# Optimization experiments

Hardware: AMD Instinct MI355X
Metric: run time of the kernel (lower is better)

## Reference

```python
import jax, jax.numpy as jnp
import numpy as np

B, SQ, SKV, D, H = 4, 2048, 2048, 1024, 16
DH = D // H  # 64


def setup_inputs() -> dict:
    key = jax.random.key(0)
    ks = jax.random.split(key, 8)
    s = 0.02  # realistic init scale for weights
    return {
        "query": jax.random.normal(ks[0], (B, SQ, D), dtype=jnp.float32),
        "value": jax.random.normal(ks[1], (B, SKV, D), dtype=jnp.float32),
        "wq": jax.random.normal(ks[2], (H, D, DH), dtype=jnp.float32) * s,
        "bq": jnp.zeros((H, DH), dtype=jnp.float32),
        "wk": jax.random.normal(ks[3], (H, D, DH), dtype=jnp.float32) * s,
        "bk": jnp.zeros((H, DH), dtype=jnp.float32),
        "wv": jax.random.normal(ks[4], (H, D, DH), dtype=jnp.float32) * s,
        "bv": jnp.zeros((H, DH), dtype=jnp.float32),
        "wo": jax.random.normal(ks[5], (D, D), dtype=jnp.float32) * s,
        "bo": jnp.zeros((D,), dtype=jnp.float32),
    }


def reference(query, value, wq, bq, wk, bk, wv, bv, wo, bo):
    # Batched equivalent of the per-head Dense loop: [B,S,D] x [H,D,DH] -> [B,H,S,DH]
    q = jnp.einsum("bsd,hde->bhse", query, wq) + bq[None, :, None, :]
    k = jnp.einsum("bsd,hde->bhse", value, wk) + bk[None, :, None, :]
    v = jnp.einsum("bsd,hde->bhse", value, wv) + bv[None, :, None, :]
    scale = 1.0 / jnp.sqrt(jnp.asarray(DH, dtype=q.dtype))
    scores = jnp.einsum("bhqe,bhke->bhqk", q, k) * scale  # [B,H,SQ,SKV]
    align = jax.nn.softmax(scores, axis=-1)
    heads = jnp.einsum("bhqk,bhke->bhqe", align, v)  # [B,H,SQ,DH]
    # concat heads along feature dim (head order preserved)
    heads = jnp.transpose(heads, (0, 2, 1, 3)).reshape(B, SQ, D)
    return heads @ wo + bo
```

## Files before the change

kernel.cpp:

```cpp
#include <hip/hip_runtime.h>
#include <stdint.h>

#define DEVI __device__ __forceinline__

typedef __bf16  bf16x8 __attribute__((ext_vector_type(8)));
typedef float   f32x4  __attribute__((ext_vector_type(4)));
typedef float   f32x16 __attribute__((ext_vector_type(16)));
typedef uint32_t u32x4 __attribute__((ext_vector_type(4)));
typedef uint32_t u32x2v __attribute__((ext_vector_type(2)));
typedef uint16_t u16x8 __attribute__((ext_vector_type(8)));
typedef uint16_t u16x4 __attribute__((ext_vector_type(4)));

static constexpr int BB = 4, SQL = 2048, SKVL = 2048, DMODEL = 1024, NH = 16;
static constexpr int MROWS = BB * SQL;
static constexpr int KD = DMODEL;

DEVI uint16_t f2bf(float x) {
  uint32_t u = __builtin_bit_cast(uint32_t, x);
  u += 0x7FFFu + ((u >> 16) & 1u);
  return (uint16_t)(u >> 16);
}
DEVI uint32_t cvt2bf(float a, float b) {
  __bf16 x = (__bf16)a, y = (__bf16)b;
  return (uint32_t)__builtin_bit_cast(uint16_t, x) |
         ((uint32_t)__builtin_bit_cast(uint16_t, y) << 16);
}
DEVI f32x4 mfma16(bf16x8 a, bf16x8 b, f32x4 c) {
  return __builtin_amdgcn_mfma_f32_16x16x32_bf16(a, b, c, 0, 0, 0);
}
DEVI f32x16 mfma32(bf16x8 a, bf16x8 b, f32x16 c) {
  return __builtin_amdgcn_mfma_f32_32x32x16_bf16(a, b, c, 0, 0, 0);
}
DEVI void gload16(const void* g, void* l) {
  __builtin_amdgcn_global_load_lds((__attribute__((address_space(1))) const void*)g,
                                   (__attribute__((address_space(3))) void*)l, 16, 0, 0);
}
DEVI bf16x8 ldread(const void* p) { return __builtin_bit_cast(bf16x8, *(const u32x4*)p); }
DEVI u32x2v plswap(uint32_t a, uint32_t b) {
  return __builtin_amdgcn_permlane32_swap(a, b, false, false);
}

__global__ __launch_bounds__(256) void k_cvt_act(const float* __restrict__ q, const float* __restrict__ v,
                                                 uint16_t* __restrict__ aq, uint16_t* __restrict__ av) {
  const int64_t n4 = (int64_t)MROWS * DMODEL / 4;
  for (int64_t i = (int64_t)blockIdx.x * 256 + threadIdx.x; i < 2 * n4; i += (int64_t)gridDim.x * 256) {
    const bool second = (i >= n4);
    const int64_t j = second ? i - n4 : i;
    const float4 x = (second ? (const float4*)v : (const float4*)q)[j];
    u16x4 o = { f2bf(x.x), f2bf(x.y), f2bf(x.z), f2bf(x.w) };
    *(u16x4*)((second ? av : aq) + j * 4) = o;
  }
}

__global__ __launch_bounds__(256) void k_cvt_w(const float* __restrict__ wq, const float* __restrict__ wk,
                                               const float* __restrict__ wv, const float* __restrict__ wo,
                                               uint16_t* __restrict__ wt) {
  const int idx = blockIdx.x * 256 + threadIdx.x;
  const int z = idx >> 20, f = idx & 1048575;
  const int n = f >> 10, d = f & 1023;
  const float* w = (z == 0) ? wq : (z == 1) ? wk : (z == 2) ? wv : wo;
  const float x = (z < 3) ? w[((n >> 6) << 16) + d * 64 + (n & 63)] : w[d * 1024 + n];
  wt[(size_t)z * 1048576 + f] = f2bf(x);
}

template <int MODE>
__global__ __launch_bounds__(256) void k_gemm(const uint16_t* __restrict__ A, const uint16_t* __restrict__ Bt,
                                              const float* __restrict__ bias, const float* __restrict__ biasB,
                                              void* __restrict__ outp, void* __restrict__ outpB,
                                              float oscale) {
  __shared__ __align__(16) uint16_t Al[128 * 64];
  __shared__ __align__(16) uint16_t Bl[128 * 64];
  const int tid = threadIdx.x;
  const int w = tid >> 6, ln = tid & 63;
  const int g = ln >> 4, lc = ln & 15;
  const int m0 = blockIdx.x * 128, n0 = blockIdx.y * 128;
  const int wm = (w >> 1) * 64, wn = (w & 1) * 64;
  const int srow = w * 32 + (ln >> 3);
  const int colp = (ln & 7) * 16;

  f32x4 acc[4][4] = {};

  for (int kt = 0; kt < KD / 64; ++kt) {
    #pragma unroll
    for (int i = 0; i < 4; ++i) {
      const int row = srow + i * 8;
      const int colb = colp ^ ((row & 7) << 4);
      gload16((const char*)(A + (size_t)(m0 + row) * KD + kt * 64) + colb,
              (char*)Al + w * 4096 + i * 1024);
      gload16((const char*)(Bt + (size_t)(n0 + row) * KD + kt * 64) + colb,
              (char*)Bl + w * 4096 + i * 1024);
    }
    __syncthreads();
    #pragma unroll
    for (int kk = 0; kk < 2; ++kk) {
      bf16x8 af[4], bfr[4];
      #pragma unroll
      for (int mt = 0; mt < 4; ++mt) {
        const int row = wm + mt * 16 + lc;
        af[mt] = ldread((const char*)Al + row * 128 + ((kk * 64 + g * 16) ^ ((row & 7) << 4)));
      }
      #pragma unroll
      for (int nt = 0; nt < 4; ++nt) {
        const int row = wn + nt * 16 + lc;
        bfr[nt] = ldread((const char*)Bl + row * 128 + ((kk * 64 + g * 16) ^ ((row & 7) << 4)));
      }
      #pragma unroll
      for (int mt = 0; mt < 4; ++mt)
        #pragma unroll
        for (int nt = 0; nt < 4; ++nt)
          acc[mt][nt] = mfma16(af[mt], bfr[nt], acc[mt][nt]);
    }
    __syncthreads();
  }
  #pragma unroll
  for (int nt = 0; nt < 4; ++nt) {
    const int n = n0 + wn + nt * 16 + lc;
    const int z = (MODE == 2) ? (n >> 10) : 0;
    const int nn = (MODE == 2) ? (n & 1023) : n;
    const float bv = (MODE == 2) ? (z ? biasB : bias)[nn] : bias[n];
    uint16_t* dst16 = (uint16_t*)((MODE == 2 && z) ? outpB : outp);
    #pragma unroll
    for (int mt = 0; mt < 4; ++mt) {
      #pragma unroll
      for (int r = 0; r < 4; ++r) {
        const int m = m0 + wm + mt * 16 + g * 4 + r;
        if (MODE != 1) {
          float val = acc[mt][nt][r] + bv;
          if (MODE == 0) val *= oscale;
          const int b = m >> 11, s = m & 2047, h = nn >> 6, e = nn & 63;
          dst16[((size_t)((b * NH + h) * SQL + s)) * 64 + e] = f2bf(val);
        } else {
          ((float*)outp)[(size_t)m * DMODEL + n] = acc[mt][nt][r] + bv;
        }
      }
    }
  }
}

__global__ __launch_bounds__(256, 2) void k_attn(const uint16_t* __restrict__ Qb,
                                                 const uint16_t* __restrict__ Kb,
                                                 const uint16_t* __restrict__ Vb,
                                                 uint16_t* __restrict__ Hd) {
  __shared__ __align__(16) uint16_t Kl[2][64 * 64];
  __shared__ __align__(16) uint16_t Vl[2][64 * 64];
  const int tid = threadIdx.x;
  const int w = tid >> 6, ln = tid & 63;
  const int ql = ln & 31, hi = ln >> 5;
  const int bh = blockIdx.y;
  const int q0 = blockIdx.x * 256 + w * 64;

  bf16x8 qf[2][4];
  #pragma unroll
  for (int qt = 0; qt < 2; ++qt) {
    const uint16_t* Qp = Qb + ((size_t)bh * SQL + q0 + qt * 32 + ql) * 64;
    #pragma unroll
    for (int s = 0; s < 4; ++s)
      qf[qt][s] = __builtin_bit_cast(bf16x8, *(const u16x8*)(Qp + s * 16 + hi * 8));
  }

  const uint16_t* Kbase = Kb + (size_t)bh * SKVL * 64;
  const uint16_t* Vbase = Vb + (size_t)bh * SKVL * 64;

  const int swl = (ln & 7) << 4;
  const int e0off = (hi << 4) ^ swl;
  const int rb = ql * 128;

  const int krow0 = w * 16 + (ln >> 3);
  const int kcolb = (((ln & 7) ^ (ln >> 3)) << 4);
  const int vkv = (tid & 31) * 2, ve0 = (tid >> 5) * 8;

  f32x16 acc[2][2] = {};
  float lsum0 = 0.f, lsum1 = 0.f;

  {
    #pragma unroll
    for (int i = 0; i < 2; ++i) {
      const int row = krow0 + i * 8;
      gload16((const char*)(Kbase + (size_t)row * 64) + kcolb,
              (char*)&Kl[0][0] + w * 2048 + i * 1024);
    }
    const u16x8 a = *(const u16x8*)(Vbase + (size_t)vkv * 64 + ve0);
    const u16x8 b = *(const u16x8*)(Vbase + (size_t)(vkv + 1) * 64 + ve0);
    #pragma unroll
    for (int i = 0; i < 8; ++i) {
      const int e = ve0 + i;
      *(uint32_t*)((char*)&Vl[0][0] + e * 128 + ((vkv * 2) ^ ((e & 7) << 4))) =
          (uint32_t)a[i] | ((uint32_t)b[i] << 16);
    }
  }
  __syncthreads();

  int cur = 0;
  for (int t = 0; t < SKVL / 64; ++t) {
    const bool pre = (t + 1 < SKVL / 64);
    u16x8 nv0, nv1;
    if (pre) {
      const uint16_t* Kc = Kbase + (size_t)(t + 1) * 4096;
      #pragma unroll
      for (int i = 0; i < 2; ++i) {
        const int row = krow0 + i * 8;
        gload16((const char*)(Kc + (size_t)row * 64) + kcolb,
                (char*)&Kl[cur ^ 1][0] + w * 2048 + i * 1024);
      }
      const uint16_t* Vc = Vbase + (size_t)(t + 1) * 4096;
      nv0 = *(const u16x8*)(Vc + (size_t)vkv * 64 + ve0);
      nv1 = *(const u16x8*)(Vc + (size_t)(vkv + 1) * 64 + ve0);
    }
    const char* Kc0 = (const char*)&Kl[cur][0];
    uint32_t w32[2][2][4][2];
    #pragma unroll
    for (int qt = 0; qt < 2; ++qt) {
      f32x16 s0 = {}, s1 = {};
      __builtin_amdgcn_s_setprio(1);
      #pragma unroll
      for (int s = 0; s < 4; ++s) {
        const int off = e0off ^ (s << 5);
        const bf16x8 k0 = ldread(Kc0 + rb + off);
        const bf16x8 k1 = ldread(Kc0 + 4096 + rb + off);
        s0 = mfma32(k0, qf[qt][s], s0);
        s1 = mfma32(k1, qf[qt][s], s1);
      }
      __builtin_amdgcn_s_setprio(0);
      float ps = 0.f;
      #pragma unroll
      for (int r = 0; r < 16; ++r) {
        s0[r] = __builtin_amdgcn_exp2f(s0[r]);
        s1[r] = __builtin_amdgcn_exp2f(s1[r]);
        ps += s0[r] + s1[r];
      }
      if (qt == 0) lsum0 += ps; else lsum1 += ps;
      #pragma unroll
      for (int c8 = 0; c8 < 4; ++c8) {
        #pragma unroll
        for (int p = 0; p < 2; ++p) {
          w32[qt][0][c8][p] = cvt2bf(s0[4 * c8 + 2 * p], s0[4 * c8 + 2 * p + 1]);
          w32[qt][1][c8][p] = cvt2bf(s1[4 * c8 + 2 * p], s1[4 * c8 + 2 * p + 1]);
        }
      }
    }
    const char* Vc0 = (const char*)&Vl[cur][0];
    __builtin_amdgcn_s_setprio(1);
    #pragma unroll
    for (int u = 0; u < 4; ++u) {
      const int tt = u >> 1, ul = u & 1;
      const int off = e0off ^ (u << 5);
      const bf16x8 v0 = ldread(Vc0 + rb + off);
      const bf16x8 v1 = ldread(Vc0 + 4096 + rb + off);
      #pragma unroll
      for (int qt = 0; qt < 2; ++qt) {
        const u32x2v e0 = plswap(w32[qt][tt][2 * ul][0], w32[qt][tt][2 * ul + 1][0]);
        const u32x2v e1 = plswap(w32[qt][tt][2 * ul][1], w32[qt][tt][2 * ul + 1][1]);
        u32x4 pj;
        pj[0] = e0[0]; pj[1] = e1[0]; pj[2] = e0[1]; pj[3] = e1[1];
        const bf16x8 pb = __builtin_bit_cast(bf16x8, pj);
        acc[qt][0] = mfma32(v0, pb, acc[qt][0]);
        acc[qt][1] = mfma32(v1, pb, acc[qt][1]);
      }
    }
    __builtin_amdgcn_s_setprio(0);
    if (pre) {
      #pragma unroll
      for (int i = 0; i < 8; ++i) {
        const int e = ve0 + i;
        *(uint32_t*)((char*)&Vl[cur ^ 1][0] + e * 128 + ((vkv * 2) ^ ((e & 7) << 4))) =
            (uint32_t)nv0[i] | ((uint32_t)nv1[i] << 16);
      }
    }
    __syncthreads();
    cur ^= 1;
  }
  const int b = bh >> 4, h = bh & 15;
  #pragma unroll
  for (int qt = 0; qt < 2; ++qt) {
    const float ls = qt ? lsum1 : lsum0;
    const float lt = ls + __shfl_xor(ls, 32);
    const float inv = __builtin_amdgcn_rcpf(lt);
    uint16_t* op = Hd + ((size_t)(b * SQL + q0 + qt * 32 + ql)) * DMODEL + h * 64;
    #pragma unroll
    for (int et = 0; et < 2; ++et) {
      #pragma unroll
      for (int r2 = 0; r2 < 8; ++r2) {
        const float v0 = acc[qt][et][2 * r2] * inv;
        const float v1 = acc[qt][et][2 * r2 + 1] * inv;
        const int e = et * 32 + 4 * hi + (r2 & 1) * 2 + (r2 >> 1) * 8;
        *(uint32_t*)(op + e) = cvt2bf(v0, v1);
      }
    }
  }
}

extern "C" void kernel_launch(void* const* d_in, const int* in_sizes, int n_in,
                              void* d_out, int out_size, void* d_ws, size_t ws_size,
                              hipStream_t stream) {
  const float* query = (const float*)d_in[0];
  const float* value = (const float*)d_in[1];
  const float* wq = (const float*)d_in[2];
  const float* bq = (const float*)d_in[3];
  const float* wk = (const float*)d_in[4];
  const float* bk = (const float*)d_in[5];
  const float* wv = (const float*)d_in[6];
  const float* bv = (const float*)d_in[7];
  const float* wo = (const float*)d_in[8];
  const float* bo = (const float*)d_in[9];

  const size_t SZ_ACT = (size_t)MROWS * DMODEL * 2;
  const size_t SZ_W   = (size_t)4 * DMODEL * DMODEL * 2;
  if (ws_size < 6 * SZ_ACT + SZ_W) return;

  char* ws = (char*)d_ws;
  uint16_t* Aq = (uint16_t*)ws;  ws += SZ_ACT;
  uint16_t* Av = (uint16_t*)ws;  ws += SZ_ACT;
  uint16_t* Wt = (uint16_t*)ws;  ws += SZ_W;
  uint16_t* Qb = (uint16_t*)ws;  ws += SZ_ACT;
  uint16_t* Kb = (uint16_t*)ws;  ws += SZ_ACT;
  uint16_t* Vb = (uint16_t*)ws;  ws += SZ_ACT;
  uint16_t* Hd = (uint16_t*)ws;  ws += SZ_ACT;

  const float QSCALE = 0.18033688011112042f;

  k_cvt_act<<<dim3(2048), dim3(256), 0, stream>>>(query, value, Aq, Av);
  k_cvt_w<<<dim3(16384), dim3(256), 0, stream>>>(wq, wk, wv, wo, Wt);
  k_gemm<0><<<dim3(64, 8), dim3(256), 0, stream>>>(Aq, Wt, bq, nullptr, Qb, nullptr, QSCALE);
  k_gemm<2><<<dim3(64, 16), dim3(256), 0, stream>>>(Av, Wt + 1048576, bk, bv, Kb, Vb, 1.0f);
  k_attn<<<dim3(8, 64), dim3(256), 0, stream>>>(Qb, Kb, Vb, Hd);
  k_gemm<1><<<dim3(64, 8), dim3(256), 0, stream>>>(Hd, Wt + 3145728, bo, nullptr, d_out, nullptr, 1.0f);
}
```

Baseline: 220.8 us.

## Split attention KV range in two and merge partials in a combine kernel

The attention kernel now splits each (batch, head) KV sequence into two halves handled by separate blocks, doubling the grid to 1024 blocks. A swizzled 1D block index groups blocks for locality. Each block writes unnormalized bf16 partial outputs and row sums to scratch reused from dead workspace buffers (Aq/Av and Wt). A new k_comb kernel adds the two partials, normalizes them and writes the head-concatenated layout. The aim is higher occupancy and more in-flight work (launch bounds raised to 4 blocks per SM), at the cost of an extra kernel launch, extra memory traffic for the partials, bf16 rounding of the partials before summing, and possible register pressure.

```diff
diff --git a/kernel.cpp b/kernel.cpp
--- a/kernel.cpp
+++ b/kernel.cpp
@@ -20,6 +20,7 @@
   u += 0x7FFFu + ((u >> 16) & 1u);
   return (uint16_t)(u >> 16);
 }
+DEVI float bf2f(uint16_t x) { return __builtin_bit_cast(float, (uint32_t)x << 16); }
 DEVI uint32_t cvt2bf(float a, float b) {
   __bf16 x = (__bf16)a, y = (__bf16)b;
   return (uint32_t)__builtin_bit_cast(uint16_t, x) |
@@ -137,17 +138,20 @@
   }
 }
 
-__global__ __launch_bounds__(256, 2) void k_attn(const uint16_t* __restrict__ Qb,
+__global__ __launch_bounds__(256, 4) void k_attn(const uint16_t* __restrict__ Qb,
                                                  const uint16_t* __restrict__ Kb,
                                                  const uint16_t* __restrict__ Vb,
-                                                 uint16_t* __restrict__ Hd) {
+                                                 uint16_t* __restrict__ Op,
+                                                 float* __restrict__ Lp) {
   __shared__ __align__(16) uint16_t Kl[2][64 * 64];
   __shared__ __align__(16) uint16_t Vl[2][64 * 64];
   const int tid = threadIdx.x;
   const int w = tid >> 6, ln = tid & 63;
   const int ql = ln & 31, hi = ln >> 5;
-  const int bh = blockIdx.y;
-  const int q0 = blockIdx.x * 256 + w * 64;
+  const int bsw = blockIdx.x;
+  const int l = (bsw & 7) * 128 + (bsw >> 3);
+  const int qx = l & 7, bh = (l >> 3) & 63, z = l >> 9;
+  const int q0 = qx * 256 + w * 64;
 
   bf16x8 qf[2][4];
   #pragma unroll
@@ -158,8 +162,8 @@
       qf[qt][s] = __builtin_bit_cast(bf16x8, *(const u16x8*)(Qp + s * 16 + hi * 8));
   }
 
-  const uint16_t* Kbase = Kb + (size_t)bh * SKVL * 64;
-  const uint16_t* Vbase = Vb + (size_t)bh * SKVL * 64;
+  const uint16_t* Kbase = Kb + ((size_t)bh * SKVL + z * 1024) * 64;
+  const uint16_t* Vbase = Vb + ((size_t)bh * SKVL + z * 1024) * 64;
 
   const int swl = (ln & 7) << 4;
   const int e0off = (hi << 4) ^ swl;
@@ -191,8 +195,8 @@
   __syncthreads();
 
   int cur = 0;
-  for (int t = 0; t < SKVL / 64; ++t) {
-    const bool pre = (t + 1 < SKVL / 64);
+  for (int t = 0; t < 16; ++t) {
+    const bool pre = (t + 1 < 16);
     u16x8 nv0, nv1;
     if (pre) {
       const uint16_t* Kc = Kbase + (size_t)(t + 1) * 4096;
@@ -269,24 +273,48 @@
     __syncthreads();
     cur ^= 1;
   }
-  const int b = bh >> 4, h = bh & 15;
   #pragma unroll
   for (int qt = 0; qt < 2; ++qt) {
     const float ls = qt ? lsum1 : lsum0;
     const float lt = ls + __shfl_xor(ls, 32);
-    const float inv = __builtin_amdgcn_rcpf(lt);
-    uint16_t* op = Hd + ((size_t)(b * SQL + q0 + qt * 32 + ql)) * DMODEL + h * 64;
+    const int q = q0 + qt * 32 + ql;
+    uint16_t* op = Op + ((size_t)(z * 64 + bh) * SQL + q) * 64;
     #pragma unroll
     for (int et = 0; et < 2; ++et) {
       #pragma unroll
       for (int r2 = 0; r2 < 8; ++r2) {
-        const float v0 = acc[qt][et][2 * r2] * inv;
-        const float v1 = acc[qt][et][2 * r2 + 1] * inv;
+        const float v0 = acc[qt][et][2 * r2];
+        const float v1 = acc[qt][et][2 * r2 + 1];
         const int e = et * 32 + 4 * hi + (r2 & 1) * 2 + (r2 >> 1) * 8;
         *(uint32_t*)(op + e) = cvt2bf(v0, v1);
       }
     }
-  }
+    if (hi == 0) Lp[(size_t)(z * 64 + bh) * SQL + q] = lt;
+  }
+}
+
+__global__ __launch_bounds__(256) void k_comb(const uint16_t* __restrict__ Op,
+                                              const float* __restrict__ Lp,
+                                              uint16_t* __restrict__ Hd) {
+  const int idx = blockIdx.x * 256 + threadIdx.x;
+  const int bh = idx >> 14;
+  const int q = (idx >> 3) & 2047;
+  const int e8 = (idx & 7) * 8;
+  const size_t zoff = (size_t)64 * SQL * 64;
+  const size_t base = ((size_t)bh * SQL + q) * 64 + e8;
+  const u16x8 a = *(const u16x8*)(Op + base);
+  const u16x8 c = *(const u16x8*)(Op + zoff + base);
+  const float lt = Lp[(size_t)bh * SQL + q] + Lp[(size_t)64 * SQL + (size_t)bh * SQL + q];
+  const float inv = __builtin_amdgcn_rcpf(lt);
+  u32x4 o;
+  #pragma unroll
+  for (int i = 0; i < 4; ++i) {
+    const float f0 = (bf2f(a[2 * i]) + bf2f(c[2 * i])) * inv;
+    const float f1 = (bf2f(a[2 * i + 1]) + bf2f(c[2 * i + 1])) * inv;
+    o[i] = cvt2bf(f0, f1);
+  }
+  const int b4 = bh >> 4, h = bh & 15;
+  *(u32x4*)(Hd + ((size_t)(b4 * SQL + q)) * DMODEL + h * 64 + e8) = o;
 }
 
 extern "C" void kernel_launch(void* const* d_in, const int* in_sizes, int n_in,
@@ -316,12 +344,16 @@
   uint16_t* Vb = (uint16_t*)ws;  ws += SZ_ACT;
   uint16_t* Hd = (uint16_t*)ws;  ws += SZ_ACT;
 
+  uint16_t* Op = Aq;
+  float*    Lp = (float*)Wt;
+
   const float QSCALE = 0.18033688011112042f;
 
   k_cvt_act<<<dim3(2048), dim3(256), 0, stream>>>(query, value, Aq, Av);
   k_cvt_w<<<dim3(16384), dim3(256), 0, stream>>>(wq, wk, wv, wo, Wt);
   k_gemm<0><<<dim3(64, 8), dim3(256), 0, stream>>>(Aq, Wt, bq, nullptr, Qb, nullptr, QSCALE);
   k_gemm<2><<<dim3(64, 16), dim3(256), 0, stream>>>(Av, Wt + 1048576, bk, bv, Kb, Vb, 1.0f);
-  k_attn<<<dim3(8, 64), dim3(256), 0, stream>>>(Qb, Kb, Vb, Hd);
+  k_attn<<<dim3(1024), dim3(256), 0, stream>>>(Qb, Kb, Vb, Op, Lp);
+  k_comb<<<dim3(4096), dim3(256), 0, stream>>>(Op, Lp, Hd);
   k_gemm<1><<<dim3(64, 8), dim3(256), 0, stream>>>(Hd, Wt + 3145728, bo, nullptr, d_out, nullptr, 1.0f);
 }
```

After: 567.9 us. 157% more time.
